# Kernel optimization log

Hardware: AMD Instinct MI355X
Metric: run time of the kernel (lower is better)

## Reference

```python
import jax, jax.numpy as jnp
import numpy as np

N, IN_DIM, HEADS, OUT_DIM = 4096, 128, 4, 64
NEG_INF = -9.0e15  # finite mask value, matches torch source


def setup_inputs() -> dict:
    key = jax.random.key(0)
    k1, k2, k3, k4, k5 = jax.random.split(key, 5)
    x = jax.random.normal(k1, (N, IN_DIM), dtype=jnp.float32)
    adj_mask = jax.random.bernoulli(k2, 0.1, (N, N))  # bool, j->i edges
    # xavier-uniform-ish scales
    lim_w = float(np.sqrt(6.0 / (IN_DIM + HEADS * OUT_DIM)))
    W_lin = jax.random.uniform(k3, (IN_DIM, HEADS * OUT_DIM), minval=-lim_w, maxval=lim_w, dtype=jnp.float32)
    lim_a = float(np.sqrt(6.0 / (2 * OUT_DIM + 1)))
    a_src = jax.random.uniform(k4, (OUT_DIM,), minval=-lim_a, maxval=lim_a, dtype=jnp.float32)
    a_dst = jax.random.uniform(k5, (OUT_DIM,), minval=-lim_a, maxval=lim_a, dtype=jnp.float32)
    return {"x": x, "adj_mask": adj_mask, "W_lin": W_lin, "a_src": a_src, "a_dst": a_dst}


def reference(x, adj_mask, W_lin, a_src, a_dst):
    n = x.shape[0]
    h = (x @ W_lin).reshape(n, HEADS, OUT_DIM)           # (N, H, D)
    # att(cat(h_i, h_j)) decomposes linearly: a_src.h_i + a_dst.h_j
    s_i = jnp.einsum("nhd,d->nh", h, a_src)              # (N, H) contribution of dest node i
    s_j = jnp.einsum("nhd,d->nh", h, a_dst)              # (N, H) contribution of source node j
    e = jax.nn.leaky_relu(s_i[:, None, :] + s_j[None, :, :], 0.2)  # (N, N, H)
    e = jnp.where(adj_mask[:, :, None], e, NEG_INF)
    attn = jax.nn.softmax(e, axis=1)                     # softmax over source nodes j
    out = jnp.einsum("ijh,jhd->ihd", attn, h)            # per-head aggregation
    return out.reshape(n, HEADS * OUT_DIM)               # concat=True
```

## Files before the change

kernel.cpp:

```cpp
#include <hip/hip_runtime.h>
#include <math.h>


#define N 4096
#define IN_DIM 128
#define HEADS 4
#define OUT_DIM 64
#define HD 256
#define LOG2E 1.4426950408889634f
#define PSHIFT 8.0f

typedef _Float16 f16x8 __attribute__((ext_vector_type(8)));
typedef __fp16 fp16x2 __attribute__((ext_vector_type(2)));
typedef float f32x4 __attribute__((ext_vector_type(4)));

union F16x8u { fp16x2 h2[4]; f16x8 v; };

#define WS_HB_OFF    0u
#define WS_SSRC_OFF  2097152u
#define WS_SDT_OFF   2162688u
#define WS_BITT_OFF  2228224u
#define WS_HSUMP_OFF 4325376u
#define WS_PL_OFF    4849664u
#define WS_PART_OFF  5373952u
#define WS_NEED8     (5373952u + 8u * 4194304u)

__device__ __forceinline__ float lrelu(float v) { return fmaxf(v, 0.2f * v); }

__device__ __forceinline__ unsigned pack_bytes(unsigned v) {
  return (v & 1u) | ((v >> 7) & 2u) | ((v >> 14) & 4u) | ((v >> 21) & 8u);
}

__global__ __launch_bounds__(256) void prep_k(const void* __restrict__ mraw,
                                              unsigned* __restrict__ bits_t,
                                              const float* __restrict__ x,
                                              const float* __restrict__ W,
                                              const float* __restrict__ a_src,
                                              const float* __restrict__ a_dst,
                                              _Float16* __restrict__ hb,
                                              float* __restrict__ s_src,
                                              float* __restrict__ s_dst_t,
                                              float* __restrict__ hsum_part) {
  if (blockIdx.x < 2048) {
    __shared__ int s_flag;
    if (threadIdx.x == 0) s_flag = 0;
    __syncthreads();
    const unsigned* mw = (const unsigned*)mraw;
    int bad = 0, g = 0;
    for (int i = threadIdx.x; i < 1024; i += 256) {
      unsigned v = mw[i];
      if (v & 0xFEFEFEFEu) bad = 1;
      if (v > 1u) g = 1;
    }
    if (bad || g) atomicOr(&s_flag, (bad ? 1 : 0) | (g ? 2 : 0));
    __syncthreads();
    const bool byte_fmt = ((s_flag & 1) == 0) && ((s_flag & 2) != 0);

    int w = blockIdx.x * 256 + threadIdx.x;
    unsigned ob = 0u;
    if (byte_fmt) {
      const uint4* p = (const uint4*)((const unsigned char*)mraw + (size_t)w * 32u);
      uint4 a = p[0], b = p[1];
      ob  =  pack_bytes(a.x)        | (pack_bytes(a.y) << 4)  | (pack_bytes(a.z) << 8)  | (pack_bytes(a.w) << 12);
      ob |= (pack_bytes(b.x) << 16) | (pack_bytes(b.y) << 20) | (pack_bytes(b.z) << 24) | (pack_bytes(b.w) << 28);
    } else {
      const uint4* p = (const uint4*)((const unsigned*)mraw + (size_t)w * 32u);
#pragma unroll
      for (int k = 0; k < 8; ++k) {
        uint4 v = p[k];
        ob |= (v.x ? 1u : 0u) << (4 * k);
        ob |= (v.y ? 1u : 0u) << (4 * k + 1);
        ob |= (v.z ? 1u : 0u) << (4 * k + 2);
        ob |= (v.w ? 1u : 0u) << (4 * k + 3);
      }
    }
    const int row = w >> 7, jc = w & 127;
    bits_t[((size_t)(row >> 6) * 128 + jc) * 64 + (row & 63)] = ob;
  } else {
    __shared__ float xs[8][IN_DIM];
    const int blk = blockIdx.x - 2048;
    const int i0 = blk * 8;
    const int c = threadIdx.x;

    ((float4*)&xs[0][0])[c] = ((const float4*)(x + (size_t)i0 * IN_DIM))[c];
    __syncthreads();

    float acc[8];
#pragma unroll
    for (int r = 0; r < 8; ++r) acc[r] = 0.f;

    for (int kk = 0; kk < IN_DIM / 4; ++kk) {
      const int k = kk * 4;
      float w0 = W[(size_t)(k + 0) * HD + c];
      float w1 = W[(size_t)(k + 1) * HD + c];
      float w2 = W[(size_t)(k + 2) * HD + c];
      float w3 = W[(size_t)(k + 3) * HD + c];
#pragma unroll
      for (int r = 0; r < 8; ++r) {
        float4 xv = *(const float4*)(&xs[r][k]);
        acc[r] = fmaf(xv.x, w0, fmaf(xv.y, w1, fmaf(xv.z, w2, fmaf(xv.w, w3, acc[r]))));
      }
    }

    {
      const int head = c >> 6, nt = (c >> 4) & 3, m15 = c & 15;
      const int unit = (head * 128 + (i0 >> 5)) * 4 + nt;
      const int lanep = ((i0 & 31) >> 3) * 16 + m15;
      f16x8 v;
#pragma unroll
      for (int r = 0; r < 8; ++r) v[r] = (_Float16)acc[r];
      *(f16x8*)(hb + (size_t)unit * 512 + lanep * 8) = v;
    }

    {
      float loc = 0.f;
#pragma unroll
      for (int r = 0; r < 8; ++r) loc += acc[r];
      hsum_part[(size_t)blk * HD + c] = loc;
    }

    const int hw = c >> 6, lane = c & 63;
    const float as = a_src[lane], ad = a_dst[lane];
#pragma unroll
    for (int r = 0; r < 8; ++r) {
      float vs = acc[r] * as, vd = acc[r] * ad;
#pragma unroll
      for (int off = 1; off < 64; off <<= 1) {
        vs += __shfl_xor(vs, off);
        vd += __shfl_xor(vd, off);
      }
      if (lane == 0) {
        s_src[(size_t)(i0 + r) * HEADS + hw] = vs * LOG2E;
        s_dst_t[(size_t)hw * N + (i0 + r)] = vd * LOG2E;
      }
    }
  }
}

__global__ __launch_bounds__(512, 4) void gat_aggr(const _Float16* __restrict__ hb,
                                                   const float* __restrict__ s_src,
                                                   const float* __restrict__ s_dst_t,
                                                   const unsigned* __restrict__ bits_t,
                                                   float* __restrict__ accp,
                                                   float* __restrict__ lp,
                                                   int jshift) {
  const int jsplit = 1 << jshift;
  const int jrange = N >> jshift;
  const int chunks = jrange >> 5;
  const int tid = threadIdx.x;
  const int wave = tid >> 6;
  const int lane = tid & 63;
  const int head = wave & 3;
  const int mg = wave >> 2;
  const int m15 = lane & 15;
  const int quad = lane >> 4;
  const int jq = blockIdx.x & (jsplit - 1);
  const int it = blockIdx.x >> jshift;
  const int i0 = it * 64;
  const int rA = i0 + mg * 32 + m15;
  const int rB = rA + 16;

  const float siA = s_src[(size_t)rA * HEADS + head];
  const float siB = s_src[(size_t)rB * HEADS + head];

  const unsigned* mt = bits_t + ((size_t)it * 128 + jq * chunks) * 64 + mg * 32 + m15;
  const float* sjb = s_dst_t + (size_t)head * N + jq * jrange + quad * 8;
  const _Float16* hbp = hb + ((size_t)(head * 128 + jq * chunks) * 4) * 512 + lane * 8;

  f32x4 accA0 = {0.f, 0.f, 0.f, 0.f}, accA1 = accA0, accA2 = accA0, accA3 = accA0;
  f32x4 accB0 = accA0, accB1 = accA0, accB2 = accA0, accB3 = accA0;
  float lA = 0.f, lB = 0.f;

  const int shq = quad * 8;

  for (int c = 0; c < chunks; ++c) {
    const unsigned mwA = mt[c * 64];
    const unsigned mwB = mt[c * 64 + 16];
    const float4 sa = *(const float4*)(sjb + c * 32);
    const float4 sb = *(const float4*)(sjb + c * 32 + 4);

    const f16x8 b0 = *(const f16x8*)(hbp + (size_t)(c * 4 + 0) * 512);
    const f16x8 b1 = *(const f16x8*)(hbp + (size_t)(c * 4 + 1) * 512);
    const f16x8 b2 = *(const f16x8*)(hbp + (size_t)(c * 4 + 2) * 512);
    const f16x8 b3 = *(const f16x8*)(hbp + (size_t)(c * 4 + 3) * 512);

    const unsigned wA = mwA >> shq;
    const unsigned wB = mwB >> shq;
    const float sjs[8] = {sa.x, sa.y, sa.z, sa.w, sb.x, sb.y, sb.z, sb.w};

    F16x8u uA, uB;
#pragma unroll
    for (int t2 = 0; t2 < 4; ++t2) {
      float pA[2], pB[2];
#pragma unroll
      for (int q = 0; q < 2; ++q) {
        const int t = t2 * 2 + q;
        const float sj = sjs[t];
        float vA = lrelu(siA + sj);
        float vB = lrelu(siB + sj);
        float xA = (((wA >> t) & 1u) ? vA : -1.0e38f) - PSHIFT;
        float xB = (((wB >> t) & 1u) ? vB : -1.0e38f) - PSHIFT;
        pA[q] = __builtin_amdgcn_exp2f(xA);
        pB[q] = __builtin_amdgcn_exp2f(xB);
        lA += pA[q];
        lB += pB[q];
      }
      uA.h2[t2] = __builtin_amdgcn_cvt_pkrtz(pA[0], pA[1]);
      uB.h2[t2] = __builtin_amdgcn_cvt_pkrtz(pB[0], pB[1]);
    }

    accA0 = __builtin_amdgcn_mfma_f32_16x16x32_f16(uA.v, b0, accA0, 0, 0, 0);
    accA1 = __builtin_amdgcn_mfma_f32_16x16x32_f16(uA.v, b1, accA1, 0, 0, 0);
    accA2 = __builtin_amdgcn_mfma_f32_16x16x32_f16(uA.v, b2, accA2, 0, 0, 0);
    accA3 = __builtin_amdgcn_mfma_f32_16x16x32_f16(uA.v, b3, accA3, 0, 0, 0);
    accB0 = __builtin_amdgcn_mfma_f32_16x16x32_f16(uB.v, b0, accB0, 0, 0, 0);
    accB1 = __builtin_amdgcn_mfma_f32_16x16x32_f16(uB.v, b1, accB1, 0, 0, 0);
    accB2 = __builtin_amdgcn_mfma_f32_16x16x32_f16(uB.v, b2, accB2, 0, 0, 0);
    accB3 = __builtin_amdgcn_mfma_f32_16x16x32_f16(uB.v, b3, accB3, 0, 0, 0);
  }

  lA += __shfl_xor(lA, 16); lA += __shfl_xor(lA, 32);
  lB += __shfl_xor(lB, 16); lB += __shfl_xor(lB, 32);
  if (quad == 0) {
    lp[((size_t)jq * N + rA) * HEADS + head] = lA;
    lp[((size_t)jq * N + rB) * HEADS + head] = lB;
  }

  const int colb = head * 64 + m15;
  float* oA = accp + (size_t)jq * (N * HD) + (size_t)(i0 + mg * 32 + quad * 4) * HD + colb;
  float* oB = oA + (size_t)16 * HD;
#pragma unroll
  for (int reg = 0; reg < 4; ++reg) {
    oA[(size_t)reg * HD + 0]  = accA0[reg];
    oA[(size_t)reg * HD + 16] = accA1[reg];
    oA[(size_t)reg * HD + 32] = accA2[reg];
    oA[(size_t)reg * HD + 48] = accA3[reg];
    oB[(size_t)reg * HD + 0]  = accB0[reg];
    oB[(size_t)reg * HD + 16] = accB1[reg];
    oB[(size_t)reg * HD + 32] = accB2[reg];
    oB[(size_t)reg * HD + 48] = accB3[reg];
  }
}

__global__ __launch_bounds__(256) void reduce_part(const float4* __restrict__ accp,
                                                   const float* __restrict__ lp,
                                                   const float* __restrict__ hsum_part,
                                                   float4* __restrict__ out, int jsplit) {
  const size_t idx = (size_t)blockIdx.x * 256 + threadIdx.x;
  const int row = (int)(idx >> 6);
  const int col4 = (int)(idx & 63);
  const int head = col4 >> 4;
  const size_t S = (size_t)N * HD / 4;

  float4 o = accp[idx];
  float lt = lp[(size_t)row * HEADS + head];
  for (int k = 1; k < jsplit; ++k) {
    float4 a = accp[idx + (size_t)k * S];
    o.x += a.x; o.y += a.y; o.z += a.z; o.w += a.w;
    lt += lp[((size_t)k * N + row) * HEADS + head];
  }
  if (lt == 0.f) {
    float4 hs = {0.f, 0.f, 0.f, 0.f};
    for (int b = 0; b < 512; ++b) {
      float4 t = ((const float4*)hsum_part)[(size_t)b * 64 + col4];
      hs.x += t.x; hs.y += t.y; hs.z += t.z; hs.w += t.w;
    }
    const float cst = 1.0f / (float)N;
    o.x = hs.x * cst; o.y = hs.y * cst; o.z = hs.z * cst; o.w = hs.w * cst;
  } else {
    const float inv = 1.0f / lt;
    o.x *= inv; o.y *= inv; o.z *= inv; o.w *= inv;
  }
  out[idx] = o;
}

extern "C" void kernel_launch(void* const* d_in, const int* in_sizes, int n_in,
                              void* d_out, int out_size, void* d_ws, size_t ws_size,
                              hipStream_t stream) {
  (void)in_sizes; (void)n_in; (void)out_size;
  const float* x = (const float*)d_in[0];
  const void* mask = d_in[1];
  const float* W = (const float*)d_in[2];
  const float* a_src = (const float*)d_in[3];
  const float* a_dst = (const float*)d_in[4];
  float* out = (float*)d_out;

  char* ws = (char*)d_ws;
  _Float16* hb = (_Float16*)(ws + WS_HB_OFF);
  float* s_src = (float*)(ws + WS_SSRC_OFF);
  float* s_dst_t = (float*)(ws + WS_SDT_OFF);
  unsigned* bits_t = (unsigned*)(ws + WS_BITT_OFF);
  float* hsum_part = (float*)(ws + WS_HSUMP_OFF);
  float* lp = (float*)(ws + WS_PL_OFF);
  float* accp = (float*)(ws + WS_PART_OFF);

  const int jshift = (ws_size >= (size_t)WS_NEED8) ? 3 : 1;
  const int jsplit = 1 << jshift;

  prep_k<<<2048 + N / 8, 256, 0, stream>>>(mask, bits_t, x, W, a_src, a_dst,
                                           hb, s_src, s_dst_t, hsum_part);
  gat_aggr<<<(N / 64) * jsplit, 512, 0, stream>>>(hb, s_src, s_dst_t, bits_t,
                                                  accp, lp, jshift);
  reduce_part<<<(N * HD / 4) / 256, 256, 0, stream>>>((const float4*)accp, lp, hsum_part,
                                                      (float4*)out, jsplit);
}
```

Measured before the change: 151.4 us.

## Fuse split-J aggregation and partial reduction into one kernel via LDS

Replaces the split-J aggregation kernel and its separate global-memory reduction kernel with one fused kernel. Each block takes 32 rows of one head, its 8 waves split the source range, and the per-wave partial accumulators and row sums are combined through shared memory before normalising and writing the output. This removes the large global round trip of partial accumulators (up to 8x N*HD floats) and one kernel launch. It also folds the PSHIFT offset and the leaky-relu into precomputed fmax/fma terms. The cost is a large static LDS footprint (about 64KB per block), which limits occupancy, plus a block-wide barrier before the final reduction.

```diff
diff --git a/kernel.cpp b/kernel.cpp
--- a/kernel.cpp
+++ b/kernel.cpp
@@ -21,11 +21,6 @@
 #define WS_SDT_OFF   2162688u
 #define WS_BITT_OFF  2228224u
 #define WS_HSUMP_OFF 4325376u
-#define WS_PL_OFF    4849664u
-#define WS_PART_OFF  5373952u
-#define WS_NEED8     (5373952u + 8u * 4194304u)
-
-__device__ __forceinline__ float lrelu(float v) { return fmaxf(v, 0.2f * v); }
 
 __device__ __forceinline__ unsigned pack_bytes(unsigned v) {
   return (v & 1u) | ((v >> 7) & 2u) | ((v >> 14) & 4u) | ((v >> 21) & 8u);
@@ -137,35 +132,34 @@
   }
 }
 
-__global__ __launch_bounds__(512, 4) void gat_aggr(const _Float16* __restrict__ hb,
-                                                   const float* __restrict__ s_src,
-                                                   const float* __restrict__ s_dst_t,
-                                                   const unsigned* __restrict__ bits_t,
-                                                   float* __restrict__ accp,
-                                                   float* __restrict__ lp,
-                                                   int jshift) {
-  const int jsplit = 1 << jshift;
-  const int jrange = N >> jshift;
-  const int chunks = jrange >> 5;
+__global__ __launch_bounds__(512, 4) void gat_fused(const _Float16* __restrict__ hb,
+                                                    const float* __restrict__ s_src,
+                                                    const float* __restrict__ s_dst_t,
+                                                    const unsigned* __restrict__ bits_t,
+                                                    const float* __restrict__ hsum_part,
+                                                    float4* __restrict__ out) {
+  __shared__ float red[8][32][64];
+  __shared__ float lred[8][32];
+
   const int tid = threadIdx.x;
-  const int wave = tid >> 6;
+  const int w = tid >> 6;
   const int lane = tid & 63;
-  const int head = wave & 3;
-  const int mg = wave >> 2;
   const int m15 = lane & 15;
   const int quad = lane >> 4;
-  const int jq = blockIdx.x & (jsplit - 1);
-  const int it = blockIdx.x >> jshift;
-  const int i0 = it * 64;
-  const int rA = i0 + mg * 32 + m15;
+  const int head = blockIdx.x >> 7;
+  const int rb = blockIdx.x & 127;
+  const int i0 = rb * 32;
+  const int rA = i0 + m15;
   const int rB = rA + 16;
 
   const float siA = s_src[(size_t)rA * HEADS + head];
   const float siB = s_src[(size_t)rB * HEADS + head];
-
-  const unsigned* mt = bits_t + ((size_t)it * 128 + jq * chunks) * 64 + mg * 32 + m15;
-  const float* sjb = s_dst_t + (size_t)head * N + jq * jrange + quad * 8;
-  const _Float16* hbp = hb + ((size_t)(head * 128 + jq * chunks) * 4) * 512 + lane * 8;
+  const float siAa = siA - PSHIFT, siAb = 0.2f * siA - PSHIFT;
+  const float siBa = siB - PSHIFT, siBb = 0.2f * siB - PSHIFT;
+
+  const unsigned* mt = bits_t + ((size_t)(rb >> 1) * 128 + w * 16) * 64 + (i0 & 32) + m15;
+  const float* sjb = s_dst_t + (size_t)head * N + w * 512 + quad * 8;
+  const _Float16* hbp = hb + ((size_t)(head * 128 + w * 16) * 4) * 512 + lane * 8;
 
   f32x4 accA0 = {0.f, 0.f, 0.f, 0.f}, accA1 = accA0, accA2 = accA0, accA3 = accA0;
   f32x4 accB0 = accA0, accB1 = accA0, accB2 = accA0, accB3 = accA0;
@@ -173,7 +167,7 @@
 
   const int shq = quad * 8;
 
-  for (int c = 0; c < chunks; ++c) {
+  for (int c = 0; c < 16; ++c) {
     const unsigned mwA = mt[c * 64];
     const unsigned mwB = mt[c * 64 + 16];
     const float4 sa = *(const float4*)(sjb + c * 32);
@@ -196,10 +190,10 @@
       for (int q = 0; q < 2; ++q) {
         const int t = t2 * 2 + q;
         const float sj = sjs[t];
-        float vA = lrelu(siA + sj);
-        float vB = lrelu(siB + sj);
-        float xA = (((wA >> t) & 1u) ? vA : -1.0e38f) - PSHIFT;
-        float xB = (((wB >> t) & 1u) ? vB : -1.0e38f) - PSHIFT;
+        const float mA = fmaxf(siAa + sj, fmaf(0.2f, sj, siAb));
+        const float mB = fmaxf(siBa + sj, fmaf(0.2f, sj, siBb));
+        const float xA = (((wA >> t) & 1u) ? mA : -1.0e38f);
+        const float xB = (((wB >> t) & 1u) ? mB : -1.0e38f);
         pA[q] = __builtin_amdgcn_exp2f(xA);
         pB[q] = __builtin_amdgcn_exp2f(xB);
         lA += pA[q];
@@ -222,48 +216,39 @@
   lA += __shfl_xor(lA, 16); lA += __shfl_xor(lA, 32);
   lB += __shfl_xor(lB, 16); lB += __shfl_xor(lB, 32);
   if (quad == 0) {
-    lp[((size_t)jq * N + rA) * HEADS + head] = lA;
-    lp[((size_t)jq * N + rB) * HEADS + head] = lB;
-  }
-
-  const int colb = head * 64 + m15;
-  float* oA = accp + (size_t)jq * (N * HD) + (size_t)(i0 + mg * 32 + quad * 4) * HD + colb;
-  float* oB = oA + (size_t)16 * HD;
+    lred[w][m15] = lA;
+    lred[w][16 + m15] = lB;
+  }
+
 #pragma unroll
   for (int reg = 0; reg < 4; ++reg) {
-    oA[(size_t)reg * HD + 0]  = accA0[reg];
-    oA[(size_t)reg * HD + 16] = accA1[reg];
-    oA[(size_t)reg * HD + 32] = accA2[reg];
-    oA[(size_t)reg * HD + 48] = accA3[reg];
-    oB[(size_t)reg * HD + 0]  = accB0[reg];
-    oB[(size_t)reg * HD + 16] = accB1[reg];
-    oB[(size_t)reg * HD + 32] = accB2[reg];
-    oB[(size_t)reg * HD + 48] = accB3[reg];
-  }
-}
-
-__global__ __launch_bounds__(256) void reduce_part(const float4* __restrict__ accp,
-                                                   const float* __restrict__ lp,
-                                                   const float* __restrict__ hsum_part,
-                                                   float4* __restrict__ out, int jsplit) {
-  const size_t idx = (size_t)blockIdx.x * 256 + threadIdx.x;
-  const int row = (int)(idx >> 6);
-  const int col4 = (int)(idx & 63);
-  const int head = col4 >> 4;
-  const size_t S = (size_t)N * HD / 4;
-
-  float4 o = accp[idx];
-  float lt = lp[(size_t)row * HEADS + head];
-  for (int k = 1; k < jsplit; ++k) {
-    float4 a = accp[idx + (size_t)k * S];
-    o.x += a.x; o.y += a.y; o.z += a.z; o.w += a.w;
-    lt += lp[((size_t)k * N + row) * HEADS + head];
+    const int ra = quad * 4 + reg;
+    red[w][ra][m15 +  0] = accA0[reg];
+    red[w][ra][m15 + 16] = accA1[reg];
+    red[w][ra][m15 + 32] = accA2[reg];
+    red[w][ra][m15 + 48] = accA3[reg];
+    red[w][16 + ra][m15 +  0] = accB0[reg];
+    red[w][16 + ra][m15 + 16] = accB1[reg];
+    red[w][16 + ra][m15 + 32] = accB2[reg];
+    red[w][16 + ra][m15 + 48] = accB3[reg];
+  }
+  __syncthreads();
+
+  const int row = tid >> 4;
+  const int c4 = tid & 15;
+  float4 o = {0.f, 0.f, 0.f, 0.f};
+  float lt = 0.f;
+#pragma unroll
+  for (int k = 0; k < 8; ++k) {
+    const float4 v = *(const float4*)&red[k][row][c4 * 4];
+    o.x += v.x; o.y += v.y; o.z += v.z; o.w += v.w;
+    lt += lred[k][row];
   }
   if (lt == 0.f) {
     float4 hs = {0.f, 0.f, 0.f, 0.f};
     for (int b = 0; b < 512; ++b) {
-      float4 t = ((const float4*)hsum_part)[(size_t)b * 64 + col4];
-      hs.x += t.x; hs.y += t.y; hs.z += t.z; hs.w += t.w;
+      float4 t4 = ((const float4*)hsum_part)[(size_t)b * 64 + head * 16 + c4];
+      hs.x += t4.x; hs.y += t4.y; hs.z += t4.z; hs.w += t4.w;
     }
     const float cst = 1.0f / (float)N;
     o.x = hs.x * cst; o.y = hs.y * cst; o.z = hs.z * cst; o.w = hs.w * cst;
@@ -271,13 +256,13 @@
     const float inv = 1.0f / lt;
     o.x *= inv; o.y *= inv; o.z *= inv; o.w *= inv;
   }
-  out[idx] = o;
+  out[(size_t)(i0 + row) * 64 + head * 16 + c4] = o;
 }
 
 extern "C" void kernel_launch(void* const* d_in, const int* in_sizes, int n_in,
                               void* d_out, int out_size, void* d_ws, size_t ws_size,
                               hipStream_t stream) {
-  (void)in_sizes; (void)n_in; (void)out_size;
+  (void)in_sizes; (void)n_in; (void)out_size; (void)ws_size;
   const float* x = (const float*)d_in[0];
   const void* mask = d_in[1];
   const float* W = (const float*)d_in[2];
@@ -291,16 +276,9 @@
   float* s_dst_t = (float*)(ws + WS_SDT_OFF);
   unsigned* bits_t = (unsigned*)(ws + WS_BITT_OFF);
   float* hsum_part = (float*)(ws + WS_HSUMP_OFF);
-  float* lp = (float*)(ws + WS_PL_OFF);
-  float* accp = (float*)(ws + WS_PART_OFF);
-
-  const int jshift = (ws_size >= (size_t)WS_NEED8) ? 3 : 1;
-  const int jsplit = 1 << jshift;
 
   prep_k<<<2048 + N / 8, 256, 0, stream>>>(mask, bits_t, x, W, a_src, a_dst,
                                            hb, s_src, s_dst_t, hsum_part);
-  gat_aggr<<<(N / 64) * jsplit, 512, 0, stream>>>(hb, s_src, s_dst_t, bits_t,
-                                                  accp, lp, jshift);
-  reduce_part<<<(N * HD / 4) / 256, 256, 0, stream>>>((const float4*)accp, lp, hsum_part,
-                                                      (float4*)out, jsplit);
-}
+  gat_fused<<<512, 512, 0, stream>>>(hb, s_src, s_dst_t, bits_t, hsum_part,
+                                     (float4*)out);
+}
```

Result: faster. 141.0 us (-6.9%).
